# Kernel optimization log

Hardware: AMD Instinct MI355X
Metric: run time of the kernel (lower is better)

The kernel has to match this reference:

```python
import jax, jax.numpy as jnp
import numpy as np

NUM_CLASSES = 81
SCORE_THRESH = 0.05
BBOX_XFORM_CLIP = float(np.log(1000.0 / 16.0))
WX, WY, WW, WH = 10.0, 10.0, 5.0, 5.0           # post-processor box_coder weights


def setup_inputs() -> dict:
    key = jax.random.key(0)
    ks = jax.random.split(key, 10)
    R, C, P, H = 2000, 256, 7, 1024
    D = C * P * P  # 12544
    x = jax.random.normal(ks[0], (R, C, P, P), jnp.float32)
    xy = jax.random.uniform(ks[1], (R, 2), jnp.float32) * 600.0
    wh = jax.random.uniform(ks[2], (R, 2), jnp.float32) * 200.0 + 1.0
    boxes = jnp.concatenate([xy, xy + wh], axis=1)  # valid xyxy proposals
    s = 0.01
    W6 = jax.random.normal(ks[3], (D, H), jnp.float32) * s
    b6 = jnp.zeros((H,), jnp.float32)
    W7 = jax.random.normal(ks[4], (H, H), jnp.float32) * s
    b7 = jnp.zeros((H,), jnp.float32)
    Wcls = jax.random.normal(ks[5], (H, NUM_CLASSES), jnp.float32) * s
    bcls = jnp.zeros((NUM_CLASSES,), jnp.float32)
    Wbox = jax.random.normal(ks[6], (H, NUM_CLASSES * 4), jnp.float32) * s
    bbox_b = jnp.zeros((NUM_CLASSES * 4,), jnp.float32)
    return {"x": x, "boxes": boxes, "W6": W6, "b6": b6, "W7": W7, "b7": b7,
            "Wcls": Wcls, "bcls": bcls, "Wbox": Wbox, "bbox_b": bbox_b}


def _decode(reg, boxes):
    w = boxes[:, 2] - boxes[:, 0] + 1.0
    h = boxes[:, 3] - boxes[:, 1] + 1.0
    cx = boxes[:, 0] + 0.5 * w
    cy = boxes[:, 1] + 0.5 * h
    dx = reg[..., 0] / WX
    dy = reg[..., 1] / WY
    dw = jnp.minimum(reg[..., 2] / WW, BBOX_XFORM_CLIP)
    dh = jnp.minimum(reg[..., 3] / WH, BBOX_XFORM_CLIP)
    pcx = dx * w[:, None] + cx[:, None]
    pcy = dy * h[:, None] + cy[:, None]
    pw = jnp.exp(dw) * w[:, None]
    ph = jnp.exp(dh) * h[:, None]
    return jnp.stack([pcx - 0.5 * pw, pcy - 0.5 * ph,
                      pcx + 0.5 * pw - 1.0, pcy + 0.5 * ph - 1.0], axis=-1)


def reference(x, boxes, W6, b6, W7, b7, Wcls, bcls, Wbox, bbox_b):
    R = x.shape[0]
    f = x.reshape(R, -1)                          # [R, 12544]
    f6 = jax.nn.relu(f @ W6 + b6)                 # roi_output, [R, 1024]
    f7 = jax.nn.relu(f6 @ W7 + b7)                # [R, 1024]
    probs = jax.nn.softmax(f7 @ Wcls + bcls, axis=-1)       # [R, 81]
    reg = (f7 @ Wbox + bbox_b).reshape(R, NUM_CLASSES, 4)   # [R, 81, 4]
    dec = _decode(reg, boxes)                     # [R, 81, 4]
    # per_class_extend, fixed-shape: drop background class 0, mask below threshold
    pj = probs[:, 1:]                             # [R, 80]
    bj = dec[:, 1:, :]                            # [R, 80, 4]
    keep = pj > SCORE_THRESH
    scores_m = jnp.where(keep, pj, 0.0)
    boxes_m = jnp.where(keep[..., None], bj, 0.0).reshape(R, -1)  # [R, 320]
    return jnp.concatenate([scores_m, boxes_m, f6], axis=-1)      # [R, 1424]
```

## Files before the change

### kernel.cpp

```cpp
#include <hip/hip_runtime.h>
#include <stdint.h>

typedef float f32x4 __attribute__((ext_vector_type(4)));
typedef __bf16 bf16x8 __attribute__((ext_vector_type(8)));
typedef unsigned short us4 __attribute__((ext_vector_type(4)));

__device__ __forceinline__ unsigned short f32_to_bf16(float f) {
  union { float f; uint32_t u; } v; v.f = f;
  return (unsigned short)((v.u + 0x7FFFu + ((v.u >> 16) & 1u)) >> 16);
}

__device__ __forceinline__ void gload16(const void* g, void* l) {
  __builtin_amdgcn_global_load_lds((const __attribute__((address_space(1))) void*)g,
                                   (__attribute__((address_space(3))) void*)l, 16, 0, 0);
}

template <int EPI>
__global__ __launch_bounds__(256, 2) void gemm_bf16(
    const unsigned short* __restrict__ A, const unsigned short* __restrict__ Bt,
    int M, int NB, int K, int Mtiles, int Ntiles, int splits,
    float* __restrict__ outF, unsigned short* __restrict__ outH,
    const float* __restrict__ bias, const float* __restrict__ bias2,
    int NV, size_t splitStride)
{
  __shared__ unsigned short lds[8192];
  const int tid = threadIdx.x;
  const int lane = tid & 63;
  const int wave = tid >> 6;

  int bid = blockIdx.x;
  const int mt = bid % Mtiles; bid /= Mtiles;
  const int nt = bid % Ntiles; bid /= Ntiles;
  const int sp = bid;

  const int nK = K >> 5;
  const int chunk = nK / splits;
  const int kBegin = sp * chunk;
  const int kEnd = kBegin + chunk;

  const int rowl = tid & 127;
  const int k8l = tid >> 7;
  int aRow = mt * 128 + rowl; if (aRow > M - 1) aRow = M - 1;
  int bRow = nt * 128 + rowl; if (bRow > NB - 1) bRow = NB - 1;
  const unsigned short* gA = A + (size_t)aRow * K + k8l * 8;
  const unsigned short* gB = Bt + (size_t)bRow * K + k8l * 8;
  unsigned short* lA1 = &lds[(size_t)tid * 8];
  unsigned short* lA2 = &lds[((size_t)tid + 256) * 8];
  unsigned short* lB1 = &lds[4096 + (size_t)tid * 8];
  unsigned short* lB2 = &lds[4096 + ((size_t)tid + 256) * 8];

  const int k8 = lane >> 4;
  const int rsel = lane & 15;
  const int wrBase = (wave >> 1) * 64;
  const int wcBase = (wave & 1) * 64;
  int aOff[4], bOff[4];
#pragma unroll
  for (int m = 0; m < 4; ++m) aOff[m] = (k8 * 128 + wrBase + m * 16 + rsel) * 8;
#pragma unroll
  for (int n = 0; n < 4; ++n) bOff[n] = 4096 + (k8 * 128 + wcBase + n * 16 + rsel) * 8;

  f32x4 acc[4][4];
  const f32x4 zero = {0.f, 0.f, 0.f, 0.f};
#pragma unroll
  for (int m = 0; m < 4; ++m)
#pragma unroll
    for (int n = 0; n < 4; ++n) acc[m][n] = zero;

  for (int kt = kBegin; kt < kEnd; ++kt) {
    const unsigned short* a = gA + kt * 32;
    const unsigned short* b = gB + kt * 32;
    gload16(a, lA1);
    gload16(a + 16, lA2);
    gload16(b, lB1);
    gload16(b + 16, lB2);
    __syncthreads();
    bf16x8 af[4], bfv[4];
#pragma unroll
    for (int m = 0; m < 4; ++m) af[m] = *(const bf16x8*)&lds[aOff[m]];
#pragma unroll
    for (int n = 0; n < 4; ++n) bfv[n] = *(const bf16x8*)&lds[bOff[n]];
#pragma unroll
    for (int m = 0; m < 4; ++m)
#pragma unroll
      for (int n = 0; n < 4; ++n)
        acc[m][n] = __builtin_amdgcn_mfma_f32_16x16x32_bf16(af[m], bfv[n], acc[m][n], 0, 0, 0);
    __syncthreads();
  }

  const int colBase = nt * 128 + wcBase + rsel;
  const int rowBase = mt * 128 + wrBase + (lane >> 4) * 4;
#pragma unroll
  for (int m = 0; m < 4; ++m) {
#pragma unroll
    for (int n = 0; n < 4; ++n) {
      const int col = colBase + n * 16;
#pragma unroll
      for (int j = 0; j < 4; ++j) {
        const int row = rowBase + m * 16 + j;
        if (row < M) {
          float v = acc[m][n][j];
          if (EPI == 0) {
            outF[sp * splitStride + (size_t)row * 1024 + col] = v;
          } else if (EPI == 1) {
            v += bias[col];
            v = fmaxf(v, 0.f);
            outH[(size_t)row * 1024 + col] = f32_to_bf16(v);
          } else {
            if (col < NV) {
              v += (col < 81) ? bias[col] : bias2[col - 81];
              outF[(size_t)row * NV + col] = v;
            }
          }
        }
      }
    }
  }
}

__global__ void transpose_to_bf16(const float* __restrict__ src, unsigned short* __restrict__ dst,
                                  int R, int C, int dstRowOff, int dstLd) {
  __shared__ float tile[32][33];
  const int c0 = blockIdx.x * 32, r0 = blockIdx.y * 32;
  const int tx = threadIdx.x, ty = threadIdx.y;
#pragma unroll
  for (int i = ty; i < 32; i += 8) {
    int r = r0 + i, c = c0 + tx;
    tile[i][tx] = (r < R && c < C) ? src[(size_t)r * C + c] : 0.f;
  }
  __syncthreads();
#pragma unroll
  for (int i = ty; i < 32; i += 8) {
    int c = c0 + i, r = r0 + tx;
    if (c < C && r < R) dst[(size_t)(dstRowOff + c) * dstLd + r] = f32_to_bf16(tile[tx][i]);
  }
}

__global__ void convert_to_bf16(const float* __restrict__ src, unsigned short* __restrict__ dst,
                                long n4) {
  for (long i = blockIdx.x * (long)blockDim.x + threadIdx.x; i < n4;
       i += (long)gridDim.x * blockDim.x) {
    f32x4 v = *(const f32x4*)(src + i * 4);
    us4 h;
#pragma unroll
    for (int j = 0; j < 4; ++j) h[j] = f32_to_bf16(v[j]);
    *(us4*)(dst + i * 4) = h;
  }
}

__global__ void reduce_bias_relu(const float* __restrict__ Cp, int splits, size_t sstride,
                                 const float* __restrict__ b6, float* __restrict__ out,
                                 unsigned short* __restrict__ f6b, int M) {
  const long total = (long)M * 256;
  for (long i = blockIdx.x * (long)blockDim.x + threadIdx.x; i < total;
       i += (long)gridDim.x * blockDim.x) {
    const long row = i >> 8;
    const int c4 = (int)(i & 255) * 4;
    const size_t off = ((size_t)row << 10) + c4;
    f32x4 s = *(const f32x4*)(Cp + off);
    for (int sp = 1; sp < splits; ++sp) s += *(const f32x4*)(Cp + (size_t)sp * sstride + off);
    s += *(const f32x4*)(b6 + c4);
    us4 h;
#pragma unroll
    for (int j = 0; j < 4; ++j) { s[j] = fmaxf(s[j], 0.f); h[j] = f32_to_bf16(s[j]); }
    *(f32x4*)(out + (size_t)row * 1424 + 400 + c4) = s;
    *(us4*)(f6b + off) = h;
  }
}

__global__ void head_epilogue(const float* __restrict__ cb, const float* __restrict__ boxes,
                              float* __restrict__ out, int M) {
  const float CLIP = 4.135166556742356f;
  const int row = blockIdx.x * 4 + (threadIdx.x >> 6);
  const int lane = threadIdx.x & 63;
  if (row >= M) return;
  const float* L = cb + (size_t)row * 405;
  const float v0 = L[lane];
  const float v1 = (lane < 17) ? L[64 + lane] : -1e30f;
  float mx = fmaxf(v0, v1);
#pragma unroll
  for (int off = 32; off; off >>= 1) mx = fmaxf(mx, __shfl_xor(mx, off, 64));
  float e0 = __expf(v0 - mx);
  float e1 = (lane < 17) ? __expf(v1 - mx) : 0.f;
  float sum = e0 + e1;
#pragma unroll
  for (int off = 32; off; off >>= 1) sum += __shfl_xor(sum, off, 64);
  const float inv = 1.f / sum;

  const float bx0 = boxes[row * 4 + 0], by0 = boxes[row * 4 + 1];
  const float bx1 = boxes[row * 4 + 2], by1 = boxes[row * 4 + 3];
  const float w = bx1 - bx0 + 1.f, h = by1 - by0 + 1.f;
  const float cx = bx0 + 0.5f * w, cy = by0 + 0.5f * h;
  float* orow = out + (size_t)row * 1424;

#pragma unroll
  for (int t = 0; t < 2; ++t) {
    const int c = (t == 0) ? lane : 64 + lane;
    const bool valid = (t == 0) ? (lane >= 1) : (lane < 17);
    if (valid) {
      const float p = ((t == 0) ? e0 : e1) * inv;
      const float* rg = L + 81 + c * 4;
      const float dx = rg[0] * 0.1f, dy = rg[1] * 0.1f;
      const float dw = fminf(rg[2] * 0.2f, CLIP), dh = fminf(rg[3] * 0.2f, CLIP);
      const float pcx = dx * w + cx, pcy = dy * h + cy;
      const float pw = __expf(dw) * w, ph = __expf(dh) * h;
      const bool keep = p > 0.05f;
      orow[c - 1] = keep ? p : 0.f;
      float* ob = orow + 80 + (c - 1) * 4;
      ob[0] = keep ? (pcx - 0.5f * pw) : 0.f;
      ob[1] = keep ? (pcy - 0.5f * ph) : 0.f;
      ob[2] = keep ? (pcx + 0.5f * pw - 1.f) : 0.f;
      ob[3] = keep ? (pcy + 0.5f * ph - 1.f) : 0.f;
    }
  }
}

extern "C" void kernel_launch(void* const* d_in, const int* in_sizes, int n_in,
                              void* d_out, int out_size, void* d_ws, size_t ws_size,
                              hipStream_t stream) {
  const float* x     = (const float*)d_in[0];
  const float* boxes = (const float*)d_in[1];
  const float* W6    = (const float*)d_in[2];
  const float* b6    = (const float*)d_in[3];
  const float* W7    = (const float*)d_in[4];
  const float* b7    = (const float*)d_in[5];
  const float* Wcls  = (const float*)d_in[6];
  const float* bcls  = (const float*)d_in[7];
  const float* Wbox  = (const float*)d_in[8];
  const float* bboxb = (const float*)d_in[9];
  float* out = (float*)d_out;

  const int M = 2000, D = 12544, H = 1024;
  char* p = (char*)d_ws;
  auto carve = [&](size_t bytes) { char* r = p; p += (bytes + 255) & ~(size_t)255; return r; };
  unsigned short* xb   = (unsigned short*)carve((size_t)M * D * 2);
  unsigned short* W6T  = (unsigned short*)carve((size_t)H * D * 2);
  unsigned short* W7T  = (unsigned short*)carve((size_t)H * H * 2);
  unsigned short* WcbT = (unsigned short*)carve((size_t)405 * H * 2);
  unsigned short* f6b  = (unsigned short*)carve((size_t)M * H * 2);
  unsigned short* f7b  = (unsigned short*)carve((size_t)M * H * 2);
  float* cbv           = (float*)carve((size_t)M * 405 * 4);
  size_t used = (size_t)(p - (char*)d_ws);
  size_t remain = (ws_size > used) ? ws_size - used : 0;
  int splits = 4;
  while (splits > 1 && (size_t)splits * M * H * 4 + 1024 > remain) splits >>= 1;
  float* Cp = (float*)carve((size_t)splits * M * H * 4);

  convert_to_bf16<<<4096, 256, 0, stream>>>(x, xb, (long)M * D / 4);
  transpose_to_bf16<<<dim3(32, 392), dim3(32, 8), 0, stream>>>(W6, W6T, D, H, 0, D);
  transpose_to_bf16<<<dim3(32, 32), dim3(32, 8), 0, stream>>>(W7, W7T, H, H, 0, H);
  transpose_to_bf16<<<dim3(3, 32), dim3(32, 8), 0, stream>>>(Wcls, WcbT, H, 81, 0, H);
  transpose_to_bf16<<<dim3(11, 32), dim3(32, 8), 0, stream>>>(Wbox, WcbT, H, 324, 81, H);

  gemm_bf16<0><<<16 * 8 * splits, 256, 0, stream>>>(xb, W6T, M, H, D, 16, 8, splits,
                                                    Cp, nullptr, nullptr, nullptr, 0,
                                                    (size_t)M * H);
  reduce_bias_relu<<<2048, 256, 0, stream>>>(Cp, splits, (size_t)M * H, b6, out, f6b, M);

  gemm_bf16<1><<<16 * 8, 256, 0, stream>>>(f6b, W7T, M, H, H, 16, 8, 1,
                                           nullptr, f7b, b7, nullptr, 0, 0);

  gemm_bf16<2><<<16 * 4, 256, 0, stream>>>(f7b, WcbT, M, 405, H, 16, 4, 1,
                                           cbv, nullptr, bcls, bboxb, 405, 0);

  head_epilogue<<<(M + 3) / 4, 256, 0, stream>>>(cbv, boxes, out, M);
}
```

Measured before the change: 419.4 us.

## Double-buffer GEMM LDS tiles, vectorize weight transpose, raise split-K to eight

The GEMM loop now issues the global-to-LDS loads for the next K tile into a second LDS buffer while the MFMAs run on the current one. The goal is to hide load latency behind compute, at the cost of doubling LDS per block. The weight transpose switches to 64x64 tiles with float4 reads, in-LDS bf16 conversion and 4-wide stores, to cut memory transactions. Split-K for the first GEMM rises from 4 to 8 to use more CUs, which adds partial-sum traffic and more work for the reduce step.

```diff
diff --git a/kernel.cpp b/kernel.cpp
--- a/kernel.cpp
+++ b/kernel.cpp
@@ -23,7 +23,7 @@
     const float* __restrict__ bias, const float* __restrict__ bias2,
     int NV, size_t splitStride)
 {
-  __shared__ unsigned short lds[8192];
+  __shared__ unsigned short lds[16384];
   const int tid = threadIdx.x;
   const int lane = tid & 63;
   const int wave = tid >> 6;
@@ -44,10 +44,6 @@
   int bRow = nt * 128 + rowl; if (bRow > NB - 1) bRow = NB - 1;
   const unsigned short* gA = A + (size_t)aRow * K + k8l * 8;
   const unsigned short* gB = Bt + (size_t)bRow * K + k8l * 8;
-  unsigned short* lA1 = &lds[(size_t)tid * 8];
-  unsigned short* lA2 = &lds[((size_t)tid + 256) * 8];
-  unsigned short* lB1 = &lds[4096 + (size_t)tid * 8];
-  unsigned short* lB2 = &lds[4096 + ((size_t)tid + 256) * 8];
 
   const int k8 = lane >> 4;
   const int rsel = lane & 15;
@@ -66,25 +62,34 @@
 #pragma unroll
     for (int n = 0; n < 4; ++n) acc[m][n] = zero;
 
+  auto stage = [&](int kt, int b) {
+    const unsigned short* a = gA + kt * 32;
+    const unsigned short* bsrc = gB + kt * 32;
+    unsigned short* base = &lds[b * 8192];
+    gload16(a,         base + tid * 8);
+    gload16(a + 16,    base + (tid + 256) * 8);
+    gload16(bsrc,      base + 4096 + tid * 8);
+    gload16(bsrc + 16, base + 4096 + (tid + 256) * 8);
+  };
+
+  stage(kBegin, 0);
+  __syncthreads();
+  int cur = 0;
   for (int kt = kBegin; kt < kEnd; ++kt) {
-    const unsigned short* a = gA + kt * 32;
-    const unsigned short* b = gB + kt * 32;
-    gload16(a, lA1);
-    gload16(a + 16, lA2);
-    gload16(b, lB1);
-    gload16(b + 16, lB2);
-    __syncthreads();
+    if (kt + 1 < kEnd) stage(kt + 1, cur ^ 1);
+    const int cbase = cur * 8192;
     bf16x8 af[4], bfv[4];
 #pragma unroll
-    for (int m = 0; m < 4; ++m) af[m] = *(const bf16x8*)&lds[aOff[m]];
-#pragma unroll
-    for (int n = 0; n < 4; ++n) bfv[n] = *(const bf16x8*)&lds[bOff[n]];
+    for (int m = 0; m < 4; ++m) af[m] = *(const bf16x8*)&lds[cbase + aOff[m]];
+#pragma unroll
+    for (int n = 0; n < 4; ++n) bfv[n] = *(const bf16x8*)&lds[cbase + bOff[n]];
 #pragma unroll
     for (int m = 0; m < 4; ++m)
 #pragma unroll
       for (int n = 0; n < 4; ++n)
         acc[m][n] = __builtin_amdgcn_mfma_f32_16x16x32_bf16(af[m], bfv[n], acc[m][n], 0, 0, 0);
     __syncthreads();
+    cur ^= 1;
   }
 
   const int colBase = nt * 128 + wcBase + rsel;
@@ -119,19 +124,40 @@
 
 __global__ void transpose_to_bf16(const float* __restrict__ src, unsigned short* __restrict__ dst,
                                   int R, int C, int dstRowOff, int dstLd) {
-  __shared__ float tile[32][33];
-  const int c0 = blockIdx.x * 32, r0 = blockIdx.y * 32;
-  const int tx = threadIdx.x, ty = threadIdx.y;
-#pragma unroll
-  for (int i = ty; i < 32; i += 8) {
-    int r = r0 + i, c = c0 + tx;
-    tile[i][tx] = (r < R && c < C) ? src[(size_t)r * C + c] : 0.f;
+  __shared__ unsigned short tile[64][66];
+  const int c0 = blockIdx.x * 64, r0 = blockIdx.y * 64;
+  const int t = threadIdx.x;
+  const bool fast = ((C & 3) == 0) && (c0 + 64 <= C);
+  const int lr0 = t >> 4;
+  const int lc4 = (t & 15) * 4;
+#pragma unroll
+  for (int i = 0; i < 4; ++i) {
+    const int lr = lr0 + i * 16;
+    const size_t rowOff = (size_t)(r0 + lr) * C;
+    if (fast) {
+      f32x4 v = *(const f32x4*)(src + rowOff + c0 + lc4);
+#pragma unroll
+      for (int j = 0; j < 4; ++j) tile[lr][lc4 + j] = f32_to_bf16(v[j]);
+    } else {
+#pragma unroll
+      for (int j = 0; j < 4; ++j) {
+        const int c = c0 + lc4 + j;
+        tile[lr][lc4 + j] = (c < C) ? f32_to_bf16(src[rowOff + c]) : (unsigned short)0;
+      }
+    }
   }
   __syncthreads();
-#pragma unroll
-  for (int i = ty; i < 32; i += 8) {
-    int c = c0 + i, r = r0 + tx;
-    if (c < C && r < R) dst[(size_t)(dstRowOff + c) * dstLd + r] = f32_to_bf16(tile[tx][i]);
+  const int kk = (t & 15) * 4;
+#pragma unroll
+  for (int i = 0; i < 4; ++i) {
+    const int lc = lr0 + i * 16;
+    const int c = c0 + lc;
+    if (c < C) {
+      us4 h;
+#pragma unroll
+      for (int j = 0; j < 4; ++j) h[j] = tile[kk + j][lc];
+      *(us4*)(dst + (size_t)(dstRowOff + c) * dstLd + r0 + kk) = h;
+    }
   }
 }
 
@@ -240,16 +266,15 @@
   unsigned short* f7b  = (unsigned short*)carve((size_t)M * H * 2);
   float* cbv           = (float*)carve((size_t)M * 405 * 4);
   size_t used = (size_t)(p - (char*)d_ws);
-  size_t remain = (ws_size > used) ? ws_size - used : 0;
-  int splits = 4;
-  while (splits > 1 && (size_t)splits * M * H * 4 + 1024 > remain) splits >>= 1;
+  int splits = 8;
+  while (splits > 1 && used + (size_t)splits * M * H * 4 + 1024 > ws_size) splits >>= 1;
   float* Cp = (float*)carve((size_t)splits * M * H * 4);
 
   convert_to_bf16<<<4096, 256, 0, stream>>>(x, xb, (long)M * D / 4);
-  transpose_to_bf16<<<dim3(32, 392), dim3(32, 8), 0, stream>>>(W6, W6T, D, H, 0, D);
-  transpose_to_bf16<<<dim3(32, 32), dim3(32, 8), 0, stream>>>(W7, W7T, H, H, 0, H);
-  transpose_to_bf16<<<dim3(3, 32), dim3(32, 8), 0, stream>>>(Wcls, WcbT, H, 81, 0, H);
-  transpose_to_bf16<<<dim3(11, 32), dim3(32, 8), 0, stream>>>(Wbox, WcbT, H, 324, 81, H);
+  transpose_to_bf16<<<dim3(16, 196), 256, 0, stream>>>(W6, W6T, D, H, 0, D);
+  transpose_to_bf16<<<dim3(16, 16), 256, 0, stream>>>(W7, W7T, H, H, 0, H);
+  transpose_to_bf16<<<dim3(2, 16), 256, 0, stream>>>(Wcls, WcbT, H, 81, 0, H);
+  transpose_to_bf16<<<dim3(6, 16), 256, 0, stream>>>(Wbox, WcbT, H, 324, 81, H);
 
   gemm_bf16<0><<<16 * 8 * splits, 256, 0, stream>>>(xb, W6T, M, H, D, 16, 8, splits,
                                                     Cp, nullptr, nullptr, nullptr, 0,
```

Measured after the change: 424.7 us. About the same (+1.3%).
